# Optimization experiments

Hardware: AMD Instinct MI355X
Metric: run time of the kernel (lower is better)

## Reference

```python
import jax, jax.numpy as jnp
import numpy as np

B, C, CI, H, W = 16, 256, 128, 64, 64


def setup_inputs() -> dict:
    key = jax.random.key(0)
    k1, k2, k3, k4, k5, k6 = jax.random.split(key, 6)
    x_gallery = jax.random.normal(k1, (B, C, H, W), dtype=jnp.float32)
    x_query = jax.random.normal(k2, (B, C, H, W), dtype=jnp.float32)
    # 1x1 conv weights (kernel_size=1 -> equivalent to per-pixel linear map)
    s = 1.0 / np.sqrt(C)
    theta_w = jax.random.uniform(k3, (CI, C), jnp.float32, -s, s)
    theta_b = jax.random.uniform(k4, (CI,), jnp.float32, -s, s)
    phi_w = jax.random.uniform(k5, (CI, C), jnp.float32, -s, s)
    phi_b = jax.random.uniform(k6, (CI,), jnp.float32, -s, s)
    return {"x_gallery": x_gallery, "x_query": x_query,
            "theta_w": theta_w, "theta_b": theta_b,
            "phi_w": phi_w, "phi_b": phi_b}


def reference(x_gallery, x_query, theta_w, theta_b, phi_w, phi_b):
    b, c, h, w = x_gallery.shape
    # 1x1 convs == channel-mixing einsum
    theta_x = jnp.einsum('bchw,oc->bohw', x_gallery, theta_w) + theta_b[None, :, None, None]
    phi_x = jnp.einsum('bchw,oc->bohw', x_query, phi_w) + phi_b[None, :, None, None]
    t = theta_x.reshape(b, theta_x.shape[1], -1)   # [B, CI, HW]
    p = phi_x.reshape(b, phi_x.shape[1], -1)       # [B, CI, H'W']
    n = p.shape[-1]
    # f[b, i, j] = <theta[:, i], phi[:, j]> / N   (norm == 'size')
    f = jnp.einsum('bci,bcj->bij', t, p) / n       # [B, HW, H'W']
    f = jnp.max(f, axis=2)                         # row-wise max (non-softmax attention)
    f = f.reshape(b, 1, h, w)
    return jax.nn.sigmoid(f)                       # message == 'attention_map'
```

## Files before the change

### kernel.cpp

```cpp
#include <hip/hip_runtime.h>
#include <hip/hip_bf16.h>

#define B_   16
#define CIN  256
#define CO   128
#define HW   4096

typedef __attribute__((ext_vector_type(8))) short short8;
typedef __attribute__((ext_vector_type(4))) float f32x4;

__device__ __forceinline__ short f32_to_bf16_rne(float f) {
    union { float f; unsigned u; } v; v.f = f;
    unsigned u = v.u;
    u += 0x7fffu + ((u >> 16) & 1u);
    return (short)(u >> 16);
}

__global__ __launch_bounds__(256) void wconv_kernel(
    const float* __restrict__ tw, const float* __restrict__ pw,
    short* __restrict__ wbf)
{
    const int idx = blockIdx.x * 256 + threadIdx.x;
    const float v = (idx < CO * CIN) ? tw[idx] : pw[idx - CO * CIN];
    wbf[idx] = f32_to_bf16_rne(v);
}

__global__ __launch_bounds__(256, 3) void proj_kernel(
    const float* __restrict__ xg, const float* __restrict__ xq,
    const float* __restrict__ tb, const float* __restrict__ pb,
    const short* __restrict__ wbf,
    short* __restrict__ tT, short* __restrict__ pT)
{
    const int n     = blockIdx.x;
    const int xcd   = n & 7;
    const int q     = n >> 3;
    const int b     = xcd + 8 * (q & 1);
    const int r2    = q >> 1;
    const int which = r2 & 1;
    const int itile = r2 >> 1;

    const float* x    = which ? xq : xg;
    const float* bias = which ? pb : tb;
    const short* wb   = wbf + which * CO * CIN;
    short*       out  = which ? pT : tT;

    const int i0   = itile * 64;
    const int tid  = threadIdx.x;
    const int lane = tid & 63;
    const int wv   = tid >> 6;
    const int nrow = lane & 15;
    const int quad = lane >> 4;

    const int col4 = tid & 15;
    const int rp   = tid >> 4;

    __shared__ short xT[2][64][72];

    f32x4 acc[4][2] = {};

    float bias_v[2];
    bias_v[0] = bias[wv * 32 + 0  + nrow];
    bias_v[1] = bias[wv * 32 + 16 + nrow];

    short8 wfrag[4][2][2];
    #pragma unroll
    for (int c4 = 0; c4 < 4; c4++)
        #pragma unroll
        for (int ks = 0; ks < 2; ks++)
            #pragma unroll
            for (int nt = 0; nt < 2; nt++)
                wfrag[c4][ks][nt] = *(const short8*)(
                    wb + (wv * 32 + nt * 16 + nrow) * CIN + c4 * 64 + ks * 32 + quad * 8);

    const float* xb = x + (long)b * CIN * HW + i0;

    float4 cva[2], cvb[2];

    auto load_chunk = [&](int cc) {
        #pragma unroll
        for (int rr = 0; rr < 2; rr++) {
            const int row = rr * 32 + rp * 2;
            cva[rr] = *(const float4*)(xb + (long)(cc + row)     * HW + col4 * 4);
            cvb[rr] = *(const float4*)(xb + (long)(cc + row + 1) * HW + col4 * 4);
        }
    };
    auto store_chunk = [&](int buf) {
        #pragma unroll
        for (int rr = 0; rr < 2; rr++) {
            const int row = rr * 32 + rp * 2;
            const float* pa  = (const float*)&cva[rr];
            const float* pb2 = (const float*)&cvb[rr];
            #pragma unroll
            for (int k = 0; k < 4; k++) {
                const unsigned lo = (unsigned short)f32_to_bf16_rne(pa[k]);
                const unsigned hi = (unsigned short)f32_to_bf16_rne(pb2[k]);
                *(unsigned*)&xT[buf][col4 * 4 + k][row] = lo | (hi << 16);
            }
        }
    };
    auto mfma_chunk = [&](int c4, int buf) {
        #pragma unroll
        for (int ks = 0; ks < 2; ks++)
            #pragma unroll
            for (int mt = 0; mt < 4; mt++) {
                const short8 a = *(const short8*)&xT[buf][mt * 16 + nrow][ks * 32 + quad * 8];
                acc[mt][0] = __builtin_amdgcn_mfma_f32_16x16x32_bf16(a, wfrag[c4][ks][0], acc[mt][0], 0, 0, 0);
                acc[mt][1] = __builtin_amdgcn_mfma_f32_16x16x32_bf16(a, wfrag[c4][ks][1], acc[mt][1], 0, 0, 0);
            }
    };

    load_chunk(0);
    store_chunk(0);
    #pragma unroll
    for (int c4 = 0; c4 < 4; c4++) {
        __syncthreads();
        if (c4 < 3) load_chunk(c4 * 64 + 64);
        mfma_chunk(c4, c4 & 1);
        if (c4 < 3) store_chunk((c4 + 1) & 1);
    }

    #pragma unroll
    for (int mt = 0; mt < 4; mt++)
        #pragma unroll
        for (int nt = 0; nt < 2; nt++) {
            const int co = wv * 32 + nt * 16 + nrow;
            #pragma unroll
            for (int r = 0; r < 4; r++) {
                const int il = mt * 16 + quad * 4 + r;
                out[((long)b * HW + i0 + il) * CO + co] =
                    f32_to_bf16_rne(acc[mt][nt][r] + bias_v[nt]);
            }
        }
}

__global__ __launch_bounds__(256, 1) void maxgemm_kernel(
    const short* __restrict__ tT, const short* __restrict__ pT,
    float* __restrict__ out)
{
    const int n     = blockIdx.x;
    const int b     = (n & 7) + 8 * ((n >> 3) & 1);
    const int itile = n >> 4;
    const int i0    = itile * 256;
    const int tid   = threadIdx.x;
    const int lane  = tid & 63;
    const int wv    = tid >> 6;
    const int nrow  = lane & 15;
    const int quad  = lane >> 4;

    __shared__ short bT[2][64][128];

    short8 afrag[4][4];
    {
        const short* tb2 = tT + ((long)b * HW + i0 + wv * 64) * CO;
        #pragma unroll
        for (int mt = 0; mt < 4; mt++)
            #pragma unroll
            for (int ks = 0; ks < 4; ks++)
                afrag[mt][ks] = *(const short8*)(tb2 + (mt * 16 + nrow) * CO + ks * 32 + quad * 8);
    }

    const short* pb2 = pT + (long)b * HW * CO;
    const int sc8 = tid & 15;
    const int sj0 = tid >> 4;

    short8 sreg[4];
    auto stage_load = [&](int jt) {
        const short* src = pb2 + (long)jt * 64 * CO;
        #pragma unroll
        for (int r = 0; r < 4; r++)
            sreg[r] = *(const short8*)(src + (sj0 + r * 16) * CO + sc8 * 8);
    };
    auto stage_write = [&](int buf) {
        #pragma unroll
        for (int r = 0; r < 4; r++) {
            const int j  = sj0 + r * 16;
            const int c8 = sc8 ^ (j & 7);
            *(short8*)&bT[buf][j][c8 * 8] = sreg[r];
        }
    };

    f32x4 vmax[4];
    #pragma unroll
    for (int mt = 0; mt < 4; mt++)
        vmax[mt] = (f32x4){-1e30f, -1e30f, -1e30f, -1e30f};

    auto compute = [&](int buf) {
        #pragma unroll
        for (int nt = 0; nt < 4; nt++) {
            short8 bf[4];
            const int j = nt * 16 + nrow;
            #pragma unroll
            for (int ks = 0; ks < 4; ks++) {
                const int c8 = (ks * 4 + quad) ^ (j & 7);
                bf[ks] = *(const short8*)&bT[buf][j][c8 * 8];
            }
            #pragma unroll
            for (int mt = 0; mt < 4; mt++) {
                f32x4 acc = {0.f, 0.f, 0.f, 0.f};
                #pragma unroll
                for (int ks = 0; ks < 4; ks++)
                    acc = __builtin_amdgcn_mfma_f32_16x16x32_bf16(afrag[mt][ks], bf[ks], acc, 0, 0, 0);
                #pragma unroll
                for (int r = 0; r < 4; r++)
                    vmax[mt][r] = fmaxf(vmax[mt][r], acc[r]);
            }
        }
    };

    stage_load(0);
    stage_write(0);
    for (int jt = 0; jt < 64; jt++) {
        __syncthreads();
        if (jt < 63) stage_load(jt + 1);
        compute(jt & 1);
        if (jt < 63) stage_write((jt + 1) & 1);
    }

    #pragma unroll
    for (int mt = 0; mt < 4; mt++)
        #pragma unroll
        for (int r = 0; r < 4; r++) {
            float v = vmax[mt][r];
            #pragma unroll
            for (int m = 8; m >= 1; m >>= 1)
                v = fmaxf(v, __shfl_xor(v, m, 64));
            vmax[mt][r] = v;
        }

    if (nrow == 0) {
        #pragma unroll
        for (int mt = 0; mt < 4; mt++)
            #pragma unroll
            for (int r = 0; r < 4; r++) {
                const float v = vmax[mt][r] * (1.0f / (float)HW);
                out[(long)b * HW + i0 + wv * 64 + mt * 16 + quad * 4 + r] =
                    1.0f / (1.0f + __expf(-v));
            }
    }
}

extern "C" void kernel_launch(void* const* d_in, const int* in_sizes, int n_in,
                              void* d_out, int out_size, void* d_ws, size_t ws_size,
                              hipStream_t stream) {
    const float* xg = (const float*)d_in[0];
    const float* xq = (const float*)d_in[1];
    const float* tw = (const float*)d_in[2];
    const float* tb = (const float*)d_in[3];
    const float* pw = (const float*)d_in[4];
    const float* pb = (const float*)d_in[5];
    float* out = (float*)d_out;

    short* tT  = (short*)d_ws;
    short* pT  = tT + (size_t)B_ * HW * CO;
    short* wbf = pT + (size_t)B_ * HW * CO;

    wconv_kernel<<<(2 * CO * CIN) / 256, 256, 0, stream>>>(tw, pw, wbf);
    proj_kernel<<<B_ * (HW / 64) * 2, 256, 0, stream>>>(xg, xq, tb, pb, wbf, tT, pT);
    maxgemm_kernel<<<B_ * (HW / 256), 256, 0, stream>>>(tT, pT, out);
}
```

Measured before the change: 252.4 us.

## Enlarge max-GEMM row tile and split j range across blocks with combine kernel

Each max-GEMM block now holds 128 query rows per wave (512 per block) in registers and covers only half the j range. Per-row partial maxima go to a workspace, and a new combine kernel takes the max of both halves and applies the scale and sigmoid. Each staged B tile is reused across twice as many A rows, which halves LDS traffic per MFMA while keeping the same grid size. Two independent MFMA chains are also interleaved per step. The costs are higher register pressure from 32 A fragments plus 8 accumulators, and an extra kernel launch with a partial-max write and read.

Result: faster. 239.3 us (-5.2%).

```diff
diff --git a/kernel.cpp b/kernel.cpp
--- a/kernel.cpp
+++ b/kernel.cpp
@@ -135,12 +135,15 @@
 
 __global__ __launch_bounds__(256, 1) void maxgemm_kernel(
     const short* __restrict__ tT, const short* __restrict__ pT,
-    float* __restrict__ out)
+    float* __restrict__ pmax)
 {
     const int n     = blockIdx.x;
     const int b     = (n & 7) + 8 * ((n >> 3) & 1);
-    const int itile = n >> 4;
-    const int i0    = itile * 256;
+    const int mm    = n >> 4;
+    const int itile = mm & 7;
+    const int jhalf = mm >> 3;
+    const int i0    = itile * 512;
+    const int j0    = jhalf * 2048;
     const int tid   = threadIdx.x;
     const int lane  = tid & 63;
     const int wv    = tid >> 6;
@@ -149,17 +152,17 @@
 
     __shared__ short bT[2][64][128];
 
-    short8 afrag[4][4];
+    short8 afrag[8][4];
     {
-        const short* tb2 = tT + ((long)b * HW + i0 + wv * 64) * CO;
-        #pragma unroll
-        for (int mt = 0; mt < 4; mt++)
+        const short* ta = tT + ((long)b * HW + i0 + wv * 128) * CO;
+        #pragma unroll
+        for (int mt = 0; mt < 8; mt++)
             #pragma unroll
             for (int ks = 0; ks < 4; ks++)
-                afrag[mt][ks] = *(const short8*)(tb2 + (mt * 16 + nrow) * CO + ks * 32 + quad * 8);
-    }
-
-    const short* pb2 = pT + (long)b * HW * CO;
+                afrag[mt][ks] = *(const short8*)(ta + (mt * 16 + nrow) * CO + ks * 32 + quad * 8);
+    }
+
+    const short* pb2 = pT + (long)b * HW * CO + (long)j0 * CO;
     const int sc8 = tid & 15;
     const int sj0 = tid >> 4;
 
@@ -179,45 +182,51 @@
         }
     };
 
-    f32x4 vmax[4];
-    #pragma unroll
-    for (int mt = 0; mt < 4; mt++)
+    f32x4 vmax[8];
+    #pragma unroll
+    for (int mt = 0; mt < 8; mt++)
         vmax[mt] = (f32x4){-1e30f, -1e30f, -1e30f, -1e30f};
 
+    const f32x4 kz = {0.f, 0.f, 0.f, 0.f};
+
     auto compute = [&](int buf) {
         #pragma unroll
-        for (int nt = 0; nt < 4; nt++) {
-            short8 bf[4];
-            const int j = nt * 16 + nrow;
+        for (int np = 0; np < 2; np++) {
+            short8 bf0[4], bf1[4];
+            const int ja = np * 32 + nrow;
+            const int jb = ja + 16;
             #pragma unroll
             for (int ks = 0; ks < 4; ks++) {
-                const int c8 = (ks * 4 + quad) ^ (j & 7);
-                bf[ks] = *(const short8*)&bT[buf][j][c8 * 8];
-            }
-            #pragma unroll
-            for (int mt = 0; mt < 4; mt++) {
-                f32x4 acc = {0.f, 0.f, 0.f, 0.f};
+                bf0[ks] = *(const short8*)&bT[buf][ja][(((ks * 4 + quad) ^ (ja & 7)) * 8)];
+                bf1[ks] = *(const short8*)&bT[buf][jb][(((ks * 4 + quad) ^ (jb & 7)) * 8)];
+            }
+            #pragma unroll
+            for (int mt = 0; mt < 8; mt++) {
+                f32x4 a0 = __builtin_amdgcn_mfma_f32_16x16x32_bf16(afrag[mt][0], bf0[0], kz, 0, 0, 0);
+                f32x4 a1 = __builtin_amdgcn_mfma_f32_16x16x32_bf16(afrag[mt][0], bf1[0], kz, 0, 0, 0);
                 #pragma unroll
-                for (int ks = 0; ks < 4; ks++)
-                    acc = __builtin_amdgcn_mfma_f32_16x16x32_bf16(afrag[mt][ks], bf[ks], acc, 0, 0, 0);
+                for (int ks = 1; ks < 4; ks++) {
+                    a0 = __builtin_amdgcn_mfma_f32_16x16x32_bf16(afrag[mt][ks], bf0[ks], a0, 0, 0, 0);
+                    a1 = __builtin_amdgcn_mfma_f32_16x16x32_bf16(afrag[mt][ks], bf1[ks], a1, 0, 0, 0);
+                }
                 #pragma unroll
                 for (int r = 0; r < 4; r++)
-                    vmax[mt][r] = fmaxf(vmax[mt][r], acc[r]);
+                    vmax[mt][r] = fmaxf(fmaxf(a0[r], a1[r]), vmax[mt][r]);
             }
         }
     };
 
     stage_load(0);
     stage_write(0);
-    for (int jt = 0; jt < 64; jt++) {
+    for (int jt = 0; jt < 32; jt++) {
         __syncthreads();
-        if (jt < 63) stage_load(jt + 1);
+        if (jt < 31) stage_load(jt + 1);
         compute(jt & 1);
-        if (jt < 63) stage_write((jt + 1) & 1);
-    }
-
-    #pragma unroll
-    for (int mt = 0; mt < 4; mt++)
+        if (jt < 31) stage_write((jt + 1) & 1);
+    }
+
+    #pragma unroll
+    for (int mt = 0; mt < 8; mt++)
         #pragma unroll
         for (int r = 0; r < 4; r++) {
             float v = vmax[mt][r];
@@ -228,15 +237,21 @@
         }
 
     if (nrow == 0) {
-        #pragma unroll
-        for (int mt = 0; mt < 4; mt++)
-            #pragma unroll
-            for (int r = 0; r < 4; r++) {
-                const float v = vmax[mt][r] * (1.0f / (float)HW);
-                out[(long)b * HW + i0 + wv * 64 + mt * 16 + quad * 4 + r] =
-                    1.0f / (1.0f + __expf(-v));
-            }
-    }
+        float* pm = pmax + (size_t)jhalf * (B_ * HW) + (size_t)b * HW + i0 + wv * 128;
+        #pragma unroll
+        for (int mt = 0; mt < 8; mt++)
+            #pragma unroll
+            for (int r = 0; r < 4; r++)
+                pm[mt * 16 + quad * 4 + r] = vmax[mt][r];
+    }
+}
+
+__global__ __launch_bounds__(256) void combine_kernel(
+    const float* __restrict__ pmax, float* __restrict__ out)
+{
+    const int idx = blockIdx.x * 256 + threadIdx.x;
+    const float v = fmaxf(pmax[idx], pmax[idx + B_ * HW]) * (1.0f / (float)HW);
+    out[idx] = 1.0f / (1.0f + __expf(-v));
 }
 
 extern "C" void kernel_launch(void* const* d_in, const int* in_sizes, int n_in,
@@ -253,8 +268,10 @@
     short* tT  = (short*)d_ws;
     short* pT  = tT + (size_t)B_ * HW * CO;
     short* wbf = pT + (size_t)B_ * HW * CO;
+    float* pmax = (float*)(wbf + 2 * CO * CIN);
 
     wconv_kernel<<<(2 * CO * CIN) / 256, 256, 0, stream>>>(tw, pw, wbf);
     proj_kernel<<<B_ * (HW / 64) * 2, 256, 0, stream>>>(xg, xq, tb, pb, wbf, tT, pT);
-    maxgemm_kernel<<<B_ * (HW / 256), 256, 0, stream>>>(tT, pT, out);
-}
+    maxgemm_kernel<<<B_ * (HW / 256), 256, 0, stream>>>(tT, pT, pmax);
+    combine_kernel<<<(B_ * HW) / 256, 256, 0, stream>>>(pmax, out);
+}
```
